# Optimization experiments

Hardware: AMD Instinct MI355X
Metric: run time of the kernel (lower is better)

## Reference

```python
import jax, jax.numpy as jnp
import numpy as np

B, N, M, D = 64, 512, 512, 2
BLUR, SCALING, DIAMETER, P = 0.01, 0.9, 4.0, 2


def _eps_schedule():
    # geomloss epsilon_schedule: geometric decay of temperature eps = sigma^p
    # from diameter^p down to blur^p with ratio scaling^p.
    e = np.arange(P * np.log(DIAMETER), P * np.log(BLUR), P * np.log(SCALING))
    return np.concatenate([[DIAMETER ** P], np.exp(e), [BLUR ** P]]).astype(np.float32)


def setup_inputs() -> dict:
    key = jax.random.key(0)
    k1, k2, k3, k4, k5 = jax.random.split(key, 5)
    a = jax.random.uniform(k1, (B, N), dtype=jnp.float32)
    a = a / a.sum(-1, keepdims=True)  # probability weights of measure 1
    b = jax.random.uniform(k2, (B, M), dtype=jnp.float32)
    b = b / b.sum(-1, keepdims=True)  # probability weights of measure 2
    x = jax.random.normal(k3, (B, N, D), dtype=jnp.float32)
    y = jax.random.normal(k4, (B, M, D), dtype=jnp.float32)
    w = jax.random.uniform(k5, (B,), dtype=jnp.float32)  # per-sample weights
    return {"prob1": a, "coord1": x, "prob2": b, "coord2": y, "weights": w}


def _softmin(eps, C, h):
    # softmin_eps(C, h)_i = -eps * log sum_j exp(h_j - C_ij / eps)
    # C: [B,N,M], h: [B,M] -> [B,N]
    return -eps * jax.nn.logsumexp(h[:, None, :] - C / eps, axis=2)


def reference(prob1, coord1, prob2, coord2, weights):
    a, x, b, y = prob1, coord1, prob2, coord2
    # p=2 cost: C(x,y) = |x-y|^2 / 2 (geomloss convention)
    C_xy = 0.5 * jnp.sum((x[:, :, None, :] - y[:, None, :, :]) ** 2, axis=-1)  # [B,N,M]
    C_yx = jnp.swapaxes(C_xy, 1, 2)  # [B,M,N]
    a_log = jnp.log(a)
    b_log = jnp.log(b)

    eps_arr = jnp.asarray(_eps_schedule())
    eps0 = eps_arr[0]
    # initialization at the coarsest temperature
    f = _softmin(eps0, C_xy, b_log)  # [B,N] dual potential on x
    g = _softmin(eps0, C_yx, a_log)  # [B,M] dual potential on y

    def step(carry, eps):
        f, g = carry
        ft = _softmin(eps, C_xy, b_log + g / eps)
        gt = _softmin(eps, C_yx, a_log + f / eps)
        return (0.5 * (f + ft), 0.5 * (g + gt)), None

    (f, g), _ = jax.lax.scan(step, (f, g), eps_arr)

    # geomloss runs the loop without grad and does one last extrapolation step
    f = jax.lax.stop_gradient(f)
    g = jax.lax.stop_gradient(g)
    eps_last = jnp.float32(BLUR ** P)
    f_fin = _softmin(eps_last, C_xy, b_log + g / eps_last)
    g_fin = _softmin(eps_last, C_yx, a_log + f / eps_last)

    # OT_eps(a, b) = <a, f> + <b, g>  (debias=False)
    batch_loss = jnp.sum(a * f_fin, axis=-1) + jnp.sum(b * g_fin, axis=-1)  # [B]
    return jnp.sum(batch_loss * weights)
```

## Files before the change

kernel.cpp:

```cpp
#include <hip/hip_runtime.h>
#include <cmath>

#define B_ 64
#define NP 512

constexpr float L2E  = 1.4426950408889634f;
constexpr float LN2f = 0.6931471805599453f;

typedef float f32x2 __attribute__((ext_vector_type(2)));

struct EpsList { float e[64]; };

__device__ __forceinline__ float exp2_fast(float v) {
#if __has_builtin(__builtin_amdgcn_exp2f)
    return __builtin_amdgcn_exp2f(v);
#else
    return exp2f(v);
#endif
}
__device__ __forceinline__ float log2_fast(float v) {
#if __has_builtin(__builtin_amdgcn_logf)
    return __builtin_amdgcn_logf(v);
#else
    return log2f(v);
#endif
}
__device__ __forceinline__ f32x2 vmax2(f32x2 a, f32x2 b) {
    return __builtin_elementwise_max(a, b);
}

__global__ __launch_bounds__(256, 4) void sinkhorn_pers(
    const float* __restrict__ a, const float* __restrict__ x,
    const float* __restrict__ bb, const float* __restrict__ y,
    float* __restrict__ fA, float* __restrict__ gA,
    float* __restrict__ fB, float* __restrict__ gB,
    unsigned int* __restrict__ bar, float* __restrict__ part2,
    EpsList el, int n_eps)
{
    __shared__ float4 sd[NP];
    __shared__ float s_eps[64];
    __shared__ float swred[4];

    const int bid = blockIdx.x;
    const int b   = bid >> 4;
    const int q   = bid & 15;
    const bool gside = q >= 8;
    const int rq  = q & 7;
    const int tid = threadIdx.x;
    const int sx  = tid & 15;
    const int rowbase = rq * 64 + (tid >> 4) * 4;
    unsigned int* own_ctr  = bar + b * 64 + (gside ? 32 : 0);
    unsigned int* othr_ctr = bar + b * 64 + (gside ? 0 : 32);

    if (tid < 64) s_eps[tid] = el.e[tid];

    const float2* oc2   = (const float2*)(gside ? (x + b * NP * 2) : (y + b * NP * 2));
    const float*  oprob = gside ? (a + b * NP) : (bb + b * NP);
    float ocx[2], ocy[2], on2[2], olw[2];
    #pragma unroll
    for (int u = 0; u < 2; ++u) {
        float2 c = oc2[tid + u * 256];
        ocx[u] = c.x; ocy[u] = c.y;
        on2[u] = fmaf(c.y, c.y, c.x * c.x);
        olw[u] = L2E * logf(oprob[tid + u * 256]);
    }
    const float* mcoord = gside ? (y + b * NP * 2) : (x + b * NP * 2);
    const float* mprob  = gside ? (bb + b * NP)    : (a + b * NP);
    const float4 rc01 = *(const float4*)(mcoord + rowbase * 2);
    const float4 rc23 = *(const float4*)(mcoord + rowbase * 2 + 4);
    const float x0[4] = {rc01.x, rc01.z, rc23.x, rc23.z};
    const float x1[4] = {rc01.y, rc01.w, rc23.y, rc23.w};
    float half_n2[4];
    #pragma unroll
    for (int r = 0; r < 4; ++r) half_n2[r] = 0.5f * fmaf(x1[r], x1[r], x0[r] * x0[r]);

    float pv[4];
    const int n_pass = n_eps + 2;
    __syncthreads();

    for (int p = 0; p < n_pass; ++p) {
        const float eps = (p == 0) ? s_eps[0]
                        : (p <= n_eps ? s_eps[p - 1] : s_eps[n_eps - 1]);
        const float inv_eps = 1.0f / eps;
        const float ieL2E = inv_eps * L2E;
        const float nie   = -0.5f * ieL2E;

        {
            float* opot = (gside ? ((p & 1) ? fA : fB)
                                 : ((p & 1) ? gA : gB)) + b * NP;
            #pragma unroll
            for (int u = 0; u < 2; ++u) {
                int t = tid + u * 256;
                float pot = (p != 0)
                    ? __hip_atomic_load(opot + t, __ATOMIC_RELAXED, __HIP_MEMORY_SCOPE_AGENT)
                    : 0.0f;
                float h2 = fmaf(pot, ieL2E, olw[u]);
                sd[t] = make_float4(ocx[u], ocy[u], fmaf(nie, on2[u], h2), 0.0f);
            }
        }
        __syncthreads();

        f32x2 x0p2[2], x1p2[2], m2[2], s2[2];
        #pragma unroll
        for (int pr = 0; pr < 2; ++pr) {
            x0p2[pr] = (f32x2){x0[2 * pr] * ieL2E, x0[2 * pr + 1] * ieL2E};
            x1p2[pr] = (f32x2){x1[2 * pr] * ieL2E, x1[2 * pr + 1] * ieL2E};
            m2[pr] = (f32x2)(-INFINITY);
            s2[pr] = (f32x2)(0.0f);
        }

        #pragma unroll 1
        for (int k = 0; k < 4; ++k) {
            float4 cj[8];
            #pragma unroll
            for (int u = 0; u < 8; ++u) cj[u] = sd[128 * k + 16 * u + sx];
            #pragma unroll
            for (int pr = 0; pr < 2; ++pr) {
                f32x2 arg[8];
                #pragma unroll
                for (int u = 0; u < 8; ++u) {
                    f32x2 cx2 = cj[u].x;
                    f32x2 cy2 = cj[u].y;
                    f32x2 cs2 = cj[u].z;
                    arg[u] = x1p2[pr] * cy2 + (x0p2[pr] * cx2 + cs2);
                }
                f32x2 cm = vmax2(vmax2(vmax2(arg[0], arg[1]), vmax2(arg[2], arg[3])),
                                 vmax2(vmax2(arg[4], arg[5]), vmax2(arg[6], arg[7])));
                f32x2 mn = vmax2(m2[pr], cm);
                f32x2 dl = m2[pr] - mn;
                f32x2 e; e.x = exp2_fast(dl.x); e.y = exp2_fast(dl.y);
                s2[pr] *= e;
                #pragma unroll
                for (int u = 0; u < 8; ++u) {
                    f32x2 t = arg[u] - mn;
                    f32x2 et; et.x = exp2_fast(t.x); et.y = exp2_fast(t.y);
                    s2[pr] += et;
                }
                m2[pr] = mn;
            }
        }

        float m[4] = {m2[0].x, m2[0].y, m2[1].x, m2[1].y};
        float s[4] = {s2[0].x, s2[0].y, s2[1].x, s2[1].y};
        float val[4];
        #pragma unroll
        for (int r = 0; r < 4; ++r) {
            float mr = m[r], sr = s[r];
            #pragma unroll
            for (int d = 1; d <= 8; d <<= 1) {
                float mo = __shfl_xor(mr, d);
                float so = __shfl_xor(sr, d);
                float mt = fmaxf(mr, mo);
                sr = sr * exp2_fast(mr - mt) + so * exp2_fast(mo - mt);
                mr = mt;
            }
            val[r] = fmaf(-eps * LN2f, mr + log2_fast(sr), half_n2[r]);
        }

        if (p >= 1 && p <= n_eps) {
            #pragma unroll
            for (int r = 0; r < 4; ++r) val[r] = 0.5f * (pv[r] + val[r]);
        }
        #pragma unroll
        for (int r = 0; r < 4; ++r) pv[r] = val[r];

        if (p == n_pass - 1) break;

        if (sx == 0) {
            float* dst = (gside ? ((p & 1) ? gB : gA)
                                : ((p & 1) ? fB : fA)) + b * NP + rowbase;
            #pragma unroll
            for (int r = 0; r < 4; ++r)
                __hip_atomic_store(dst + r, val[r], __ATOMIC_RELAXED,
                                   __HIP_MEMORY_SCOPE_AGENT);
        }

        __syncthreads();
        if (tid == 0) {
            __hip_atomic_fetch_add(own_ctr, 1u, __ATOMIC_RELAXED,
                                   __HIP_MEMORY_SCOPE_AGENT);
            const unsigned int target = 8u * (unsigned int)(p + 1);
            unsigned int guard = 0;
            while (__hip_atomic_load(othr_ctr, __ATOMIC_RELAXED,
                                     __HIP_MEMORY_SCOPE_AGENT) < target) {
                __builtin_amdgcn_s_sleep(1);
                if (++guard > (1u << 20)) break;
            }
        }
        __syncthreads();
    }

    float local = 0.0f;
    if (sx == 0) {
        const float4 pr = *(const float4*)(mprob + rowbase);
        local = pr.x * pv[0] + pr.y * pv[1] + pr.z * pv[2] + pr.w * pv[3];
    }
    #pragma unroll
    for (int o = 32; o > 0; o >>= 1) local += __shfl_down(local, o);
    if ((tid & 63) == 0) swred[tid >> 6] = local;
    __syncthreads();
    if (tid == 0) part2[bid] = swred[0] + swred[1] + swred[2] + swred[3];
}

__global__ void finred_k(const float* __restrict__ part2,
                         const float* __restrict__ w, float* __restrict__ out) {
    int b = threadIdx.x;
    float s = 0.0f;
    #pragma unroll
    for (int u = 0; u < 16; ++u) s += part2[b * 16 + u];
    s *= w[b];
    #pragma unroll
    for (int o = 32; o > 0; o >>= 1) s += __shfl_down(s, o);
    if (b == 0) out[0] = s;
}

extern "C" void kernel_launch(void* const* d_in, const int* in_sizes, int n_in,
                              void* d_out, int out_size, void* d_ws, size_t ws_size,
                              hipStream_t stream) {
    const float* a  = (const float*)d_in[0];
    const float* x  = (const float*)d_in[1];
    const float* bb = (const float*)d_in[2];
    const float* y  = (const float*)d_in[3];
    const float* w  = (const float*)d_in[4];
    float* out = (float*)d_out;

    unsigned char* wsb = (unsigned char*)d_ws;
    unsigned int* bar = (unsigned int*)wsb;
    float* part2 = (float*)(wsb + 64 * 64 * 4);
    float* fA = (float*)(wsb + 64 * 64 * 4 + 1024 * 4);
    const int NB = B_ * NP;
    float* gA = fA + NB;
    float* fB = gA + NB;
    float* gB = fB + NB;

    EpsList el{};
    int n_eps = 0;
    {
        const double start = 2.0 * std::log(4.0);
        const double stop  = 2.0 * std::log(0.01);
        const double step  = 2.0 * std::log(0.9);
        el.e[n_eps++] = 16.0f;
        for (int k = 0;; ++k) {
            double v = start + (double)k * step;
            if (!(v > stop)) break;
            el.e[n_eps++] = (float)std::exp(v);
        }
        el.e[n_eps++] = (float)(0.01 * 0.01);
    }

    hipMemsetAsync(bar, 0, 64 * 64 * 4, stream);

    sinkhorn_pers<<<dim3(B_ * 16), dim3(256), 0, stream>>>(
        a, x, bb, y, fA, gA, fB, gB, bar, part2, el, n_eps);

    finred_k<<<1, 64, 0, stream>>>(part2, w, out);
}
```

Baseline: 524.9 us.

## Revert packed f32x2 math to scalar and interleave batch across blocks

Replaces the packed two-wide float vector arithmetic in the logsumexp inner loop with scalar fmaf/fmaxf code. It also remaps block index so consecutive blocks belong to different batch elements (b = bid & 63), and adjusts the final reduction's partial indexing to match. The remap changes how the per-batch cooperating blocks spread across CUs and XCDs, which affects the cost of the cross-block barrier and atomics traffic. Dropping packed math may lose dual-issue throughput on packed FMA but avoids any packing overhead the compiler adds.

Result: faster. 506.6 us (-3.5%).

```diff
diff --git a/kernel.cpp b/kernel.cpp
--- a/kernel.cpp
+++ b/kernel.cpp
@@ -6,8 +6,6 @@
 
 constexpr float L2E  = 1.4426950408889634f;
 constexpr float LN2f = 0.6931471805599453f;
-
-typedef float f32x2 __attribute__((ext_vector_type(2)));
 
 struct EpsList { float e[64]; };
 
@@ -24,9 +22,6 @@
 #else
     return log2f(v);
 #endif
-}
-__device__ __forceinline__ f32x2 vmax2(f32x2 a, f32x2 b) {
-    return __builtin_elementwise_max(a, b);
 }
 
 __global__ __launch_bounds__(256, 4) void sinkhorn_pers(
@@ -42,8 +37,8 @@
     __shared__ float swred[4];
 
     const int bid = blockIdx.x;
-    const int b   = bid >> 4;
-    const int q   = bid & 15;
+    const int b   = bid & 63;
+    const int q   = bid >> 6;
     const bool gside = q >= 8;
     const int rq  = q & 7;
     const int tid = threadIdx.x;
@@ -100,13 +95,13 @@
         }
         __syncthreads();
 
-        f32x2 x0p2[2], x1p2[2], m2[2], s2[2];
+        float x0p[4], x1p[4], m[4], s[4];
         #pragma unroll
-        for (int pr = 0; pr < 2; ++pr) {
-            x0p2[pr] = (f32x2){x0[2 * pr] * ieL2E, x0[2 * pr + 1] * ieL2E};
-            x1p2[pr] = (f32x2){x1[2 * pr] * ieL2E, x1[2 * pr + 1] * ieL2E};
-            m2[pr] = (f32x2)(-INFINITY);
-            s2[pr] = (f32x2)(0.0f);
+        for (int r = 0; r < 4; ++r) {
+            x0p[r] = x0[r] * ieL2E;
+            x1p[r] = x1[r] * ieL2E;
+            m[r] = -INFINITY;
+            s[r] = 0.0f;
         }
 
         #pragma unroll 1
@@ -115,33 +110,21 @@
             #pragma unroll
             for (int u = 0; u < 8; ++u) cj[u] = sd[128 * k + 16 * u + sx];
             #pragma unroll
-            for (int pr = 0; pr < 2; ++pr) {
-                f32x2 arg[8];
+            for (int r = 0; r < 4; ++r) {
+                float arg[8];
                 #pragma unroll
-                for (int u = 0; u < 8; ++u) {
-                    f32x2 cx2 = cj[u].x;
-                    f32x2 cy2 = cj[u].y;
-                    f32x2 cs2 = cj[u].z;
-                    arg[u] = x1p2[pr] * cy2 + (x0p2[pr] * cx2 + cs2);
-                }
-                f32x2 cm = vmax2(vmax2(vmax2(arg[0], arg[1]), vmax2(arg[2], arg[3])),
-                                 vmax2(vmax2(arg[4], arg[5]), vmax2(arg[6], arg[7])));
-                f32x2 mn = vmax2(m2[pr], cm);
-                f32x2 dl = m2[pr] - mn;
-                f32x2 e; e.x = exp2_fast(dl.x); e.y = exp2_fast(dl.y);
-                s2[pr] *= e;
+                for (int u = 0; u < 8; ++u)
+                    arg[u] = fmaf(x1p[r], cj[u].y, fmaf(x0p[r], cj[u].x, cj[u].z));
+                float cm = fmaxf(fmaxf(fmaxf(arg[0], arg[1]), fmaxf(arg[2], arg[3])),
+                                 fmaxf(fmaxf(arg[4], arg[5]), fmaxf(arg[6], arg[7])));
+                float mn = fmaxf(m[r], cm);
+                s[r] *= exp2_fast(m[r] - mn);
                 #pragma unroll
-                for (int u = 0; u < 8; ++u) {
-                    f32x2 t = arg[u] - mn;
-                    f32x2 et; et.x = exp2_fast(t.x); et.y = exp2_fast(t.y);
-                    s2[pr] += et;
-                }
-                m2[pr] = mn;
-            }
-        }
-
-        float m[4] = {m2[0].x, m2[0].y, m2[1].x, m2[1].y};
-        float s[4] = {s2[0].x, s2[0].y, s2[1].x, s2[1].y};
+                for (int u = 0; u < 8; ++u) s[r] += exp2_fast(arg[u] - mn);
+                m[r] = mn;
+            }
+        }
+
         float val[4];
         #pragma unroll
         for (int r = 0; r < 4; ++r) {
@@ -207,7 +190,7 @@
     int b = threadIdx.x;
     float s = 0.0f;
     #pragma unroll
-    for (int u = 0; u < 16; ++u) s += part2[b * 16 + u];
+    for (int u = 0; u < 16; ++u) s += part2[u * 64 + b];
     s *= w[b];
     #pragma unroll
     for (int o = 32; o > 0; o >>= 1) s += __shfl_down(s, o);
```
